# Optimization experiments

Measured on AMD Instinct MI355X. Metric: run time of the kernel, lower is better.

The kernel has to match this reference:

```python
import jax, jax.numpy as jnp
import numpy as np

D = 768; H = 12; HEAD = 6; SD = 64; S1 = SD * (HEAD - 1); S2 = SD * HEAD
HID = 3072; B = 8; N = 1024
SCALE = (D // H) ** -0.5
EPS = 1e-5


def _ln(x, g, b):
    m = jnp.mean(x, axis=-1, keepdims=True)
    v = jnp.var(x, axis=-1, keepdims=True)
    return (x - m) * jax.lax.rsqrt(v + EPS) * g + b


def setup_inputs() -> dict:
    key = jax.random.key(0)
    ks = jax.random.split(key, 20)
    p = lambda k, shape, s=0.02: (jax.random.normal(k, shape, dtype=jnp.float32) * s)
    return {
        "x": jax.random.normal(ks[0], (B, N, D), dtype=jnp.float32),
        # norm1 / norm12 / norm13 (pre-attention split LayerNorms)
        "ln1a_g": jnp.ones((S1,), jnp.float32), "ln1a_b": jnp.zeros((S1,), jnp.float32),
        "ln1b_g": jnp.ones((SD,), jnp.float32), "ln1b_b": jnp.zeros((SD,), jnp.float32),
        "ln1c_g": jnp.ones((D - S2,), jnp.float32), "ln1c_b": jnp.zeros((D - S2,), jnp.float32),
        # norm2 / norm22 / norm23 (pre-MLP split LayerNorms)
        "ln2a_g": jnp.ones((S1,), jnp.float32), "ln2a_b": jnp.zeros((S1,), jnp.float32),
        "ln2b_g": jnp.ones((SD,), jnp.float32), "ln2b_b": jnp.zeros((SD,), jnp.float32),
        "ln2c_g": jnp.ones((D - S2,), jnp.float32), "ln2c_b": jnp.zeros((D - S2,), jnp.float32),
        # attention (qkv has no bias since qkv_bias=False)
        "qkv_w": p(ks[1], (3 * D, D)),
        "proj_w": p(ks[2], (D, D)), "proj_b": jnp.zeros((D,), jnp.float32),
        # mlp
        "fc1_w": p(ks[3], (HID, D)), "fc1_b": jnp.zeros((HID,), jnp.float32),
        "fc2_w": p(ks[4], (D, HID)), "fc2_b": jnp.zeros((D,), jnp.float32),
    }


def _split_norm(x, ga, ba, gb, bb, gc, bc):
    return jnp.concatenate([
        _ln(x[:, :, :S1], ga, ba),
        _ln(x[:, :, S1:S2], gb, bb),
        _ln(x[:, :, S2:], gc, bc),
    ], axis=2)


def _attention(x, qkv_w, proj_w, proj_b):
    Bq, Nq, C = x.shape
    hd = C // H
    qkv = jnp.einsum('bnc,dc->bnd', x, qkv_w)  # [B,N,3C]
    qkv = qkv.reshape(Bq, Nq, 3, H, hd).transpose(2, 0, 3, 1, 4)
    q, k, v = qkv[0], qkv[1], qkv[2]  # [B,H,N,hd]
    attn = jax.nn.softmax(jnp.einsum('bhqd,bhkd->bhqk', q, k) * SCALE, axis=-1)
    y = jnp.einsum('bhqk,bhkd->bhqd', attn, v)  # [B,H,N,hd]
    y = y.transpose(0, 2, 1, 3).reshape(Bq, Nq, C)
    return jnp.einsum('bnc,dc->bnd', y, proj_w) + proj_b


def reference(x, ln1a_g, ln1a_b, ln1b_g, ln1b_b, ln1c_g, ln1c_b,
              ln2a_g, ln2a_b, ln2b_g, ln2b_b, ln2c_g, ln2c_b,
              qkv_w, proj_w, proj_b, fc1_w, fc1_b, fc2_w, fc2_b):
    norm_x = _split_norm(x, ln1a_g, ln1a_b, ln1b_g, ln1b_b, ln1c_g, ln1c_b)
    x = x + _attention(norm_x, qkv_w, proj_w, proj_b)
    norm2_x = _split_norm(x, ln2a_g, ln2a_b, ln2b_g, ln2b_b, ln2c_g, ln2c_b)
    h = jax.nn.gelu(jnp.einsum('bnc,hc->bnh', norm2_x, fc1_w) + fc1_b, approximate=False)
    x = x + (jnp.einsum('bnh,ch->bnc', h, fc2_w) + fc2_b)
    return x
```

## Files before the change

kernel.cpp:

```cpp
#include <hip/hip_runtime.h>
#include <math.h>

#define NTOK 8192
#define DIM 768
#define SEQ 1024
#define NH 12
#define HD 64
#define HID 3072
#define S1V 320
#define S2V 384

typedef unsigned short bfu;
typedef __attribute__((ext_vector_type(8))) short short8;
typedef __attribute__((ext_vector_type(4))) float f32x4;

__device__ __forceinline__ bfu f2bf(float f){
  unsigned int u = __float_as_uint(f);
  u += 0x7FFFu + ((u >> 16) & 1u);
  return (bfu)(u >> 16);
}
__device__ __forceinline__ f32x4 mfma16(short8 a, short8 b, f32x4 c){
  return __builtin_amdgcn_mfma_f32_16x16x32_bf16(a, b, c, 0, 0, 0);
}
__device__ __forceinline__ void gll16(const void* g, void* l){
  __builtin_amdgcn_global_load_lds(
      (const __attribute__((address_space(1))) unsigned int*)g,
      (__attribute__((address_space(3))) unsigned int*)l, 16, 0, 0);
}
__device__ __forceinline__ int swz(int a){ return a ^ (((a >> 7) & 7) << 4); }

__global__ __launch_bounds__(256) void cvt_kernel(const float4* __restrict__ src,
                                                  ushort4* __restrict__ dst, int n4){
  for (int i = blockIdx.x * 256 + threadIdx.x; i < n4; i += gridDim.x * 256){
    float4 f = src[i];
    ushort4 o;
    o.x = f2bf(f.x); o.y = f2bf(f.y); o.z = f2bf(f.z); o.w = f2bf(f.w);
    dst[i] = o;
  }
}

__global__ __launch_bounds__(256) void ln_split(
    const float* __restrict__ x,
    const float* __restrict__ ga, const float* __restrict__ ba,
    const float* __restrict__ gb, const float* __restrict__ bb2,
    const float* __restrict__ gc, const float* __restrict__ bc,
    bfu* __restrict__ out)
{
  const int row = blockIdx.x, t = threadIdx.x;
  const float* xr = x + (size_t)row * DIM;
  const float e0 = xr[t], e1 = xr[t + 256], e2 = xr[t + 512];
  float s0 = e0, q0 = e0 * e0, s1 = 0.f, q1 = 0.f, s2 = e2, q2 = e2 * e2;
  const int i1 = t + 256;
  if (i1 < S1V)      { s0 += e1; q0 += e1 * e1; }
  else if (i1 < S2V) { s1 += e1; q1 += e1 * e1; }
  else               { s2 += e1; q2 += e1 * e1; }
  float v[6] = {s0, q0, s1, q1, s2, q2};
  #pragma unroll
  for (int k = 0; k < 6; ++k)
    #pragma unroll
    for (int off = 32; off; off >>= 1)
      v[k] += __shfl_xor(v[k], off);
  __shared__ float red[6][4];
  const int lane = t & 63, wave = t >> 6;
  if (lane == 0){
    #pragma unroll
    for (int k = 0; k < 6; ++k) red[k][wave] = v[k];
  }
  __syncthreads();
  float tt[6];
  #pragma unroll
  for (int k = 0; k < 6; ++k) tt[k] = red[k][0] + red[k][1] + red[k][2] + red[k][3];
  const float m0 = tt[0] * (1.f/320.f);
  const float r0 = rsqrtf(tt[1] * (1.f/320.f) - m0*m0 + 1e-5f);
  const float m1 = tt[2] * (1.f/64.f);
  const float r1 = rsqrtf(tt[3] * (1.f/64.f) - m1*m1 + 1e-5f);
  const float m2 = tt[4] * (1.f/384.f);
  const float r2 = rsqrtf(tt[5] * (1.f/384.f) - m2*m2 + 1e-5f);
  bfu* orow = out + (size_t)row * DIM;
  orow[t] = f2bf((e0 - m0) * r0 * ga[t] + ba[t]);
  {
    float ov;
    if (i1 < S1V)      ov = (e1 - m0) * r0 * ga[i1] + ba[i1];
    else if (i1 < S2V) ov = (e1 - m1) * r1 * gb[i1 - S1V] + bb2[i1 - S1V];
    else               ov = (e1 - m2) * r2 * gc[i1 - S2V] + bc[i1 - S2V];
    orow[i1] = f2bf(ov);
  }
  const int i2 = t + 512;
  orow[i2] = f2bf((e2 - m2) * r2 * gc[i2 - S2V] + bc[i2 - S2V]);
}

template<int BIAS, int GELU_, int RESID, int OUTF32, int QSC>
__global__ __launch_bounds__(256) void gemm_bt(
    const bfu* __restrict__ A, const bfu* __restrict__ Bw,
    int N, int K, int ntn,
    const float* __restrict__ bias, const float* __restrict__ resid,
    float* __restrict__ outf, bfu* __restrict__ outb)
{
  __shared__ __align__(16) char lds[2][2][8192];
  const int tid = threadIdx.x;
  const int lane = tid & 63;
  const int wave = tid >> 6;
  const int wm = wave >> 1, wn = wave & 1;
  const int tm = blockIdx.x / ntn, tn = blockIdx.x % ntn;
  const int r = lane & 15, g = lane >> 4;

  f32x4 acc[4][4];
  #pragma unroll
  for (int i = 0; i < 4; ++i)
    #pragma unroll
    for (int j = 0; j < 4; ++j) acc[i][j] = (f32x4){0.f, 0.f, 0.f, 0.f};

  int rowS[2], colS[2], Pof[2];
  #pragma unroll
  for (int is = 0; is < 2; ++is){
    const int P = is * 4096 + tid * 16;
    const int L = swz(P);
    Pof[is] = P; rowS[is] = L >> 6; colS[is] = (L & 63) >> 1;
  }
  const bfu* Arow = A  + (size_t)tm * 128 * K;
  const bfu* Brow = Bw + (size_t)tn * 128 * K;

  int offA[4], offB[4];
  #pragma unroll
  for (int f = 0; f < 4; ++f){
    offA[f] = swz((wm * 64 + f * 16 + r) * 64 + g * 16);
    offB[f] = swz((wn * 64 + f * 16 + r) * 64 + g * 16);
  }

  const int nk = K >> 5;
  #pragma unroll
  for (int is = 0; is < 2; ++is){
    gll16(Arow + (size_t)rowS[is] * K + colS[is], &lds[0][0][Pof[is]]);
    gll16(Brow + (size_t)rowS[is] * K + colS[is], &lds[0][1][Pof[is]]);
  }
  __syncthreads();

  for (int t = 0; t < nk; ++t){
    const int cur = t & 1;
    if (t + 1 < nk){
      const int k0 = (t + 1) << 5;
      #pragma unroll
      for (int is = 0; is < 2; ++is){
        gll16(Arow + (size_t)rowS[is] * K + k0 + colS[is], &lds[cur ^ 1][0][Pof[is]]);
        gll16(Brow + (size_t)rowS[is] * K + k0 + colS[is], &lds[cur ^ 1][1][Pof[is]]);
      }
    }
    const char* lA = lds[cur][0];
    const char* lB = lds[cur][1];
    short8 af[4], bfv[4];
    #pragma unroll
    for (int f = 0; f < 4; ++f){
      af[f]  = *(const short8*)(lA + offA[f]);
      bfv[f] = *(const short8*)(lB + offB[f]);
    }
    #pragma unroll
    for (int i = 0; i < 4; ++i)
      #pragma unroll
      for (int j = 0; j < 4; ++j)
        acc[i][j] = mfma16(af[i], bfv[j], acc[i][j]);
    __syncthreads();
  }

  const int row0 = tm * 128 + wm * 64;
  const int col0 = tn * 128 + wn * 64;
  #pragma unroll
  for (int j = 0; j < 4; ++j){
    const int colb = col0 + j * 16 + r;
    const float bi = BIAS ? bias[colb] : 0.f;
    #pragma unroll
    for (int i = 0; i < 4; ++i){
      #pragma unroll
      for (int q = 0; q < 4; ++q){
        const int rowg = row0 + i * 16 + g * 4 + q;
        float v = acc[i][j][q] + bi;
        if (GELU_) v = 0.5f * v * (1.f + erff(v * 0.70710678118654752440f));
        if (QSC && colb < 768) v *= 0.125f;
        const size_t idx = (size_t)rowg * N + colb;
        if (RESID) v += resid[idx];
        if (OUTF32) outf[idx] = v;
        else        outb[idx] = f2bf(v);
      }
    }
  }
}

__global__ __launch_bounds__(256) void vtrans(const bfu* __restrict__ qkv, bfu* __restrict__ vt){
  __shared__ bfu tile[64][66];
  const int bh = blockIdx.x, kt = blockIdx.y;
  const int b = bh / NH, h = bh - b * NH;
  const int tid = threadIdx.x;
  const int tr = tid >> 5;
  const int tc = (tid & 31) * 2;
  #pragma unroll
  for (int pass = 0; pass < 8; ++pass){
    const int k = pass * 8 + tr;
    const bfu* src = qkv + (size_t)(b * SEQ + kt * 64 + k) * 2304 + 1536 + h * 64 + tc;
    tile[k][tc] = src[0]; tile[k][tc + 1] = src[1];
  }
  __syncthreads();
  #pragma unroll
  for (int pass = 0; pass < 8; ++pass){
    const int d = pass * 8 + tr;
    bfu* dst = vt + ((size_t)bh * 64 + d) * SEQ + kt * 64 + tc;
    dst[0] = tile[tc][d]; dst[1] = tile[tc + 1][d];
  }
}

__global__ __launch_bounds__(512) void attn2(
    const bfu* __restrict__ qkv, const bfu* __restrict__ vt, bfu* __restrict__ y)
{
  __shared__ __align__(16) char kbuf[2][8192];
  __shared__ __align__(16) char vbuf[2][8192];
  __shared__ __align__(16) char plds_all[8][2048];
  const int tid = threadIdx.x, lane = tid & 63, wave = tid >> 6;
  char* plds = plds_all[wave];
  const int blk = blockIdx.x;
  const int bh = blk >> 3, q128 = blk & 7;
  const int b = bh / NH, h = bh - b * NH;
  const int r = lane & 15, g = lane >> 4;

  const bfu* qbase = qkv + (size_t)(b * SEQ + q128 * 128 + wave * 16 + r) * 2304 + h * 64;
  const short8 qf0 = *(const short8*)(qbase + g * 8);
  const short8 qf1 = *(const short8*)(qbase + 32 + g * 8);

  const int P = tid * 16;
  const int Ls = swz(P);
  const int srow = Ls >> 7, scol = Ls & 127;
  const char* kg = (const char*)(qkv + (size_t)(b * SEQ) * 2304 + 768 + h * 64)
                   + (size_t)srow * 4608 + scol;
  const char* vg = (const char*)(vt + (size_t)bh * 64 * SEQ)
                   + (size_t)srow * 2048 + scol;

  int off[4][2];
  #pragma unroll
  for (int f = 0; f < 4; ++f){
    off[f][0] = swz((f * 16 + r) * 128 + g * 16);
    off[f][1] = swz((f * 16 + r) * 128 + 64 + g * 16);
  }

  float m_[4], l_[4];
  f32x4 yacc[4];
  #pragma unroll
  for (int i = 0; i < 4; ++i){ m_[i] = -1e30f; l_[i] = 0.f; yacc[i] = (f32x4){0.f,0.f,0.f,0.f}; }

  gll16(kg, &kbuf[0][P]);
  gll16(vg, &vbuf[0][P]);
  __syncthreads();

  for (int kt = 0; kt < 16; ++kt){
    const int cur = kt & 1;
    if (kt + 1 < 16){
      gll16(kg + (size_t)(kt + 1) * 294912, &kbuf[cur ^ 1][P]);
      gll16(vg + (kt + 1) * 128, &vbuf[cur ^ 1][P]);
    }
    const char* lK = kbuf[cur];
    const char* lV = vbuf[cur];

    f32x4 s[4];
    #pragma unroll
    for (int c = 0; c < 4; ++c){
      const short8 kf0 = *(const short8*)(lK + off[c][0]);
      const short8 kf1 = *(const short8*)(lK + off[c][1]);
      s[c] = (f32x4){0.f, 0.f, 0.f, 0.f};
      s[c] = mfma16(qf0, kf0, s[c]);
      s[c] = mfma16(qf1, kf1, s[c]);
    }
    float pm[4];
    #pragma unroll
    for (int q = 0; q < 4; ++q)
      pm[q] = fmaxf(fmaxf(s[0][q], s[1][q]), fmaxf(s[2][q], s[3][q]));
    #pragma unroll
    for (int q = 0; q < 4; ++q)
      #pragma unroll
      for (int o = 1; o < 16; o <<= 1)
        pm[q] = fmaxf(pm[q], __shfl_xor(pm[q], o));
    float rs[4];
    #pragma unroll
    for (int q = 0; q < 4; ++q){
      const float mn = fmaxf(m_[q], pm[q]);
      const float al = __expf(m_[q] - mn);
      m_[q] = mn;
      l_[q] *= al;
      #pragma unroll
      for (int f = 0; f < 4; ++f) yacc[f][q] *= al;
      float acc = 0.f;
      #pragma unroll
      for (int c = 0; c < 4; ++c){
        const float p = __expf(s[c][q] - mn);
        s[c][q] = p;
        acc += p;
      }
      rs[q] = acc;
    }
    #pragma unroll
    for (int q = 0; q < 4; ++q){
      #pragma unroll
      for (int o = 1; o < 16; o <<= 1)
        rs[q] += __shfl_xor(rs[q], o);
      l_[q] += rs[q];
    }
    #pragma unroll
    for (int c = 0; c < 4; ++c)
      #pragma unroll
      for (int q = 0; q < 4; ++q){
        const int a = swz((g * 4 + q) * 128 + (c * 16 + r) * 2);
        *(bfu*)&plds[a] = f2bf(s[c][q]);
      }
    short8 pa[2];
    #pragma unroll
    for (int ks = 0; ks < 2; ++ks)
      pa[ks] = *(const short8*)&plds[swz(r * 128 + ks * 64 + g * 16)];
    #pragma unroll
    for (int f = 0; f < 4; ++f){
      const short8 vf0 = *(const short8*)(lV + off[f][0]);
      const short8 vf1 = *(const short8*)(lV + off[f][1]);
      yacc[f] = mfma16(pa[0], vf0, yacc[f]);
      yacc[f] = mfma16(pa[1], vf1, yacc[f]);
    }
    __syncthreads();
  }

  bfu* yb = y + (size_t)(b * SEQ + q128 * 128 + wave * 16) * DIM + h * 64;
  #pragma unroll
  for (int f = 0; f < 4; ++f)
    #pragma unroll
    for (int q = 0; q < 4; ++q)
      yb[(size_t)(g * 4 + q) * DIM + f * 16 + r] = f2bf(yacc[f][q] / l_[q]);
}

extern "C" void kernel_launch(void* const* d_in, const int* in_sizes, int n_in,
                              void* d_out, int out_size, void* d_ws, size_t ws_size,
                              hipStream_t stream) {
  const float* x      = (const float*)d_in[0];
  const float* ln1ag  = (const float*)d_in[1];
  const float* ln1ab  = (const float*)d_in[2];
  const float* ln1bg  = (const float*)d_in[3];
  const float* ln1bb  = (const float*)d_in[4];
  const float* ln1cg  = (const float*)d_in[5];
  const float* ln1cb  = (const float*)d_in[6];
  const float* ln2ag  = (const float*)d_in[7];
  const float* ln2ab  = (const float*)d_in[8];
  const float* ln2bg  = (const float*)d_in[9];
  const float* ln2bb  = (const float*)d_in[10];
  const float* ln2cg  = (const float*)d_in[11];
  const float* ln2cb  = (const float*)d_in[12];
  const float* qkv_w  = (const float*)d_in[13];
  const float* proj_w = (const float*)d_in[14];
  const float* proj_b = (const float*)d_in[15];
  const float* fc1_w  = (const float*)d_in[16];
  const float* fc1_b  = (const float*)d_in[17];
  const float* fc2_w  = (const float*)d_in[18];
  const float* fc2_b  = (const float*)d_in[19];
  float* outp = (float*)d_out;

  char* ws = (char*)d_ws;
  bfu* wqkv   = (bfu*)(ws + 0);
  bfu* wproj  = (bfu*)(ws + 3538944);
  bfu* wfc1   = (bfu*)(ws + 4718592);
  bfu* wfc2   = (bfu*)(ws + 9437184);
  bfu* lnbuf  = (bfu*)(ws + 14155776);
  bfu* ybuf   = (bfu*)(ws + 26738688);
  bfu* qkvbuf = (bfu*)(ws + 39321600);
  bfu* vtbuf  = (bfu*)(ws + 77070336);
  bfu* hbuf   = qkvbuf;

  cvt_kernel<<<512, 256, 0, stream>>>((const float4*)qkv_w,  (ushort4*)wqkv, 2304*768/4);
  cvt_kernel<<<256, 256, 0, stream>>>((const float4*)proj_w, (ushort4*)wproj, 768*768/4);
  cvt_kernel<<<512, 256, 0, stream>>>((const float4*)fc1_w,  (ushort4*)wfc1, 3072*768/4);
  cvt_kernel<<<512, 256, 0, stream>>>((const float4*)fc2_w,  (ushort4*)wfc2, 768*3072/4);

  ln_split<<<NTOK, 256, 0, stream>>>(x, ln1ag, ln1ab, ln1bg, ln1bb, ln1cg, ln1cb, lnbuf);
  gemm_bt<0,0,0,0,1><<<64*18, 256, 0, stream>>>(lnbuf, wqkv, 2304, 768, 18,
                                                nullptr, nullptr, nullptr, qkvbuf);
  vtrans<<<dim3(96,16), 256, 0, stream>>>(qkvbuf, vtbuf);
  attn2<<<768, 512, 0, stream>>>(qkvbuf, vtbuf, ybuf);
  gemm_bt<1,0,1,1,0><<<64*6, 256, 0, stream>>>(ybuf, wproj, 768, 768, 6,
                                               proj_b, x, outp, nullptr);
  ln_split<<<NTOK, 256, 0, stream>>>(outp, ln2ag, ln2ab, ln2bg, ln2bb, ln2cg, ln2cb, lnbuf);
  gemm_bt<1,1,0,0,0><<<64*24, 256, 0, stream>>>(lnbuf, wfc1, 3072, 768, 24,
                                                fc1_b, nullptr, nullptr, hbuf);
  gemm_bt<1,0,1,1,0><<<64*6, 256, 0, stream>>>(hbuf, wfc2, 768, 3072, 6,
                                               fc2_b, outp, outp, nullptr);
}
```

Measured before the change: 454.4 us.

## Replace 128x128 GEMM with 256x256 tile kernel, XCD swizzle, split-K atomics for fc2

Replaces the 128x128 K=32 GEMM with a 512-thread kernel using 256x256 tiles and K=64 steps. Loads are issued two stages ahead with explicit vmcnt waits, and MFMA sections get s_setprio. Block indices are remapped across the 8 XCDs, and fc2 splits K in two and accumulates into the output with atomicAdd, relying on outp already holding the residual. This targets better data reuse and MFMA density. The risks are higher LDS and register pressure and fewer blocks, for example 96 blocks for proj, plus nondeterministic atomic float adds.

Result: slower. 503.3 us (+10.8%).

```diff
diff --git a/kernel.cpp b/kernel.cpp
--- a/kernel.cpp
+++ b/kernel.cpp
@@ -28,6 +28,7 @@
       (__attribute__((address_space(3))) unsigned int*)l, 16, 0, 0);
 }
 __device__ __forceinline__ int swz(int a){ return a ^ (((a >> 7) & 7) << 4); }
+__device__ __forceinline__ int swz2(int a){ return a ^ (((a >> 7) & 7) << 4); }
 
 __global__ __launch_bounds__(256) void cvt_kernel(const float4* __restrict__ src,
                                                   ushort4* __restrict__ dst, int n4){
@@ -89,96 +90,119 @@
   orow[i2] = f2bf((e2 - m2) * r2 * gc[i2 - S2V] + bc[i2 - S2V]);
 }
 
-template<int BIAS, int GELU_, int RESID, int OUTF32, int QSC>
-__global__ __launch_bounds__(256) void gemm_bt(
+template<int BIAS, int GELU_, int RESID, int OUTF32, int QSC, int SPLITK>
+__global__ __launch_bounds__(512, 2) void gemm256(
     const bfu* __restrict__ A, const bfu* __restrict__ Bw,
-    int N, int K, int ntn,
+    int N, int ldK, int ntn,
     const float* __restrict__ bias, const float* __restrict__ resid,
     float* __restrict__ outf, bfu* __restrict__ outb)
 {
-  __shared__ __align__(16) char lds[2][2][8192];
+  __shared__ __align__(16) char lds[2][2][32768];
   const int tid = threadIdx.x;
   const int lane = tid & 63;
   const int wave = tid >> 6;
-  const int wm = wave >> 1, wn = wave & 1;
-  const int tm = blockIdx.x / ntn, tn = blockIdx.x % ntn;
+  const int wm = wave >> 2, wn = wave & 3;
   const int r = lane & 15, g = lane >> 4;
-
-  f32x4 acc[4][4];
-  #pragma unroll
-  for (int i = 0; i < 4; ++i)
+  const int sx = (r & 7) << 4;
+
+  const int nwg = gridDim.x, cpx = nwg >> 3;
+  const int sb = (blockIdx.x & 7) * cpx + (blockIdx.x >> 3);
+  const int per = 32 * ntn;
+  const int kg  = SPLITK ? (sb / per) : 0;
+  const int rem = SPLITK ? (sb % per) : sb;
+  const int tm = rem / ntn, tn = rem % ntn;
+
+  const int Kloc = SPLITK ? (ldK >> 1) : ldK;
+  const size_t ld2 = (size_t)ldK * 2;
+  const size_t koff2 = (size_t)kg * Kloc * 2;
+
+  f32x4 acc[8][4];
+  #pragma unroll
+  for (int i = 0; i < 8; ++i)
     #pragma unroll
     for (int j = 0; j < 4; ++j) acc[i][j] = (f32x4){0.f, 0.f, 0.f, 0.f};
 
-  int rowS[2], colS[2], Pof[2];
-  #pragma unroll
-  for (int is = 0; is < 2; ++is){
-    const int P = is * 4096 + tid * 16;
-    const int L = swz(P);
-    Pof[is] = P; rowS[is] = L >> 6; colS[is] = (L & 63) >> 1;
-  }
-  const bfu* Arow = A  + (size_t)tm * 128 * K;
-  const bfu* Brow = Bw + (size_t)tn * 128 * K;
-
-  int offA[4], offB[4];
-  #pragma unroll
-  for (int f = 0; f < 4; ++f){
-    offA[f] = swz((wm * 64 + f * 16 + r) * 64 + g * 16);
-    offB[f] = swz((wn * 64 + f * 16 + r) * 64 + g * 16);
-  }
-
-  const int nk = K >> 5;
-  #pragma unroll
-  for (int is = 0; is < 2; ++is){
-    gll16(Arow + (size_t)rowS[is] * K + colS[is], &lds[0][0][Pof[is]]);
-    gll16(Brow + (size_t)rowS[is] * K + colS[is], &lds[0][1][Pof[is]]);
-  }
-  __syncthreads();
-
-  for (int t = 0; t < nk; ++t){
+  const int Ls = swz2(tid * 16);
+  const int r0 = Ls >> 7;
+  const int c0 = Ls & 127;
+  const char* Abase = (const char*)A + (size_t)tm * 256 * ld2 + koff2 + c0;
+  const char* Bbase = (const char*)Bw + (size_t)tn * 256 * ld2 + koff2 + c0;
+  const int tid16 = tid * 16;
+
+  const int nt = Kloc >> 6;
+
+  #define STAGE(b, t) do { \
+    const char* Ao = Abase + (size_t)(t) * 128; \
+    const char* Bo = Bbase + (size_t)(t) * 128; \
+    _Pragma("unroll") \
+    for (int is = 0; is < 4; ++is) \
+      gll16(Ao + (size_t)(is * 64 + r0) * ld2, &lds[b][0][is * 8192 + tid16]); \
+    _Pragma("unroll") \
+    for (int is = 0; is < 4; ++is) \
+      gll16(Bo + (size_t)(is * 64 + r0) * ld2, &lds[b][1][is * 8192 + tid16]); \
+  } while (0)
+
+  STAGE(0, 0);
+  STAGE(1, 1);
+  asm volatile("s_waitcnt vmcnt(8)" ::: "memory");
+  __builtin_amdgcn_s_barrier();
+
+  for (int t = 0; t < nt; ++t){
     const int cur = t & 1;
-    if (t + 1 < nk){
-      const int k0 = (t + 1) << 5;
-      #pragma unroll
-      for (int is = 0; is < 2; ++is){
-        gll16(Arow + (size_t)rowS[is] * K + k0 + colS[is], &lds[cur ^ 1][0][Pof[is]]);
-        gll16(Brow + (size_t)rowS[is] * K + k0 + colS[is], &lds[cur ^ 1][1][Pof[is]]);
-      }
-    }
     const char* lA = lds[cur][0];
     const char* lB = lds[cur][1];
-    short8 af[4], bfv[4];
-    #pragma unroll
-    for (int f = 0; f < 4; ++f){
-      af[f]  = *(const short8*)(lA + offA[f]);
-      bfv[f] = *(const short8*)(lB + offB[f]);
-    }
-    #pragma unroll
-    for (int i = 0; i < 4; ++i)
-      #pragma unroll
-      for (int j = 0; j < 4; ++j)
-        acc[i][j] = mfma16(af[i], bfv[j], acc[i][j]);
-    __syncthreads();
-  }
-
-  const int row0 = tm * 128 + wm * 64;
-  const int col0 = tn * 128 + wn * 64;
-  #pragma unroll
-  for (int j = 0; j < 4; ++j){
-    const int colb = col0 + j * 16 + r;
-    const float bi = BIAS ? bias[colb] : 0.f;
-    #pragma unroll
-    for (int i = 0; i < 4; ++i){
+    short8 bfr[4][2];
+    #pragma unroll
+    for (int n = 0; n < 4; ++n)
+      #pragma unroll
+      for (int h = 0; h < 2; ++h)
+        bfr[n][h] = *(const short8*)(lB + ((((wn * 64 + n * 16 + r) * 128) + h * 64 + g * 16) ^ sx));
+    #pragma unroll
+    for (int mp = 0; mp < 4; ++mp){
+      short8 afr[2][2];
+      #pragma unroll
+      for (int mm = 0; mm < 2; ++mm)
+        #pragma unroll
+        for (int h = 0; h < 2; ++h)
+          afr[mm][h] = *(const short8*)(lA + ((((wm * 128 + (mp * 2 + mm) * 16 + r) * 128) + h * 64 + g * 16) ^ sx));
+      __builtin_amdgcn_s_setprio(1);
+      #pragma unroll
+      for (int mm = 0; mm < 2; ++mm)
+        #pragma unroll
+        for (int n = 0; n < 4; ++n){
+          acc[mp * 2 + mm][n] = mfma16(afr[mm][0], bfr[n][0], acc[mp * 2 + mm][n]);
+          acc[mp * 2 + mm][n] = mfma16(afr[mm][1], bfr[n][1], acc[mp * 2 + mm][n]);
+        }
+      __builtin_amdgcn_s_setprio(0);
+    }
+    asm volatile("s_waitcnt vmcnt(0)" ::: "memory");
+    __builtin_amdgcn_s_barrier();
+    if (t + 2 < nt) STAGE(cur, t + 2);
+  }
+  #undef STAGE
+
+  const int row0 = tm * 256 + wm * 128;
+  const int col0 = tn * 256 + wn * 64;
+  #pragma unroll
+  for (int n = 0; n < 4; ++n){
+    const int colb = col0 + n * 16 + r;
+    const float bi = (BIAS && (!SPLITK || kg == 0)) ? bias[colb] : 0.f;
+    #pragma unroll
+    for (int m = 0; m < 8; ++m){
       #pragma unroll
       for (int q = 0; q < 4; ++q){
-        const int rowg = row0 + i * 16 + g * 4 + q;
-        float v = acc[i][j][q] + bi;
+        const int rowg = row0 + m * 16 + g * 4 + q;
+        float v = acc[m][n][q] + bi;
         if (GELU_) v = 0.5f * v * (1.f + erff(v * 0.70710678118654752440f));
         if (QSC && colb < 768) v *= 0.125f;
         const size_t idx = (size_t)rowg * N + colb;
-        if (RESID) v += resid[idx];
-        if (OUTF32) outf[idx] = v;
-        else        outb[idx] = f2bf(v);
+        if (SPLITK){
+          atomicAdd(&outf[idx], v);
+        } else {
+          if (RESID) v += resid[idx];
+          if (OUTF32) outf[idx] = v;
+          else        outb[idx] = f2bf(v);
+        }
       }
     }
   }
@@ -370,15 +394,15 @@
   cvt_kernel<<<512, 256, 0, stream>>>((const float4*)fc2_w,  (ushort4*)wfc2, 768*3072/4);
 
   ln_split<<<NTOK, 256, 0, stream>>>(x, ln1ag, ln1ab, ln1bg, ln1bb, ln1cg, ln1cb, lnbuf);
-  gemm_bt<0,0,0,0,1><<<64*18, 256, 0, stream>>>(lnbuf, wqkv, 2304, 768, 18,
+  gemm256<0,0,0,0,1,0><<<288, 512, 0, stream>>>(lnbuf, wqkv, 2304, 768, 9,
                                                 nullptr, nullptr, nullptr, qkvbuf);
   vtrans<<<dim3(96,16), 256, 0, stream>>>(qkvbuf, vtbuf);
   attn2<<<768, 512, 0, stream>>>(qkvbuf, vtbuf, ybuf);
-  gemm_bt<1,0,1,1,0><<<64*6, 256, 0, stream>>>(ybuf, wproj, 768, 768, 6,
+  gemm256<1,0,1,1,0,0><<<96, 512, 0, stream>>>(ybuf, wproj, 768, 768, 3,
                                                proj_b, x, outp, nullptr);
   ln_split<<<NTOK, 256, 0, stream>>>(outp, ln2ag, ln2ab, ln2bg, ln2bb, ln2cg, ln2cb, lnbuf);
-  gemm_bt<1,1,0,0,0><<<64*24, 256, 0, stream>>>(lnbuf, wfc1, 3072, 768, 24,
+  gemm256<1,1,0,0,0,0><<<384, 512, 0, stream>>>(lnbuf, wfc1, 3072, 768, 12,
                                                 fc1_b, nullptr, nullptr, hbuf);
-  gemm_bt<1,0,1,1,0><<<64*6, 256, 0, stream>>>(hbuf, wfc2, 768, 3072, 6,
-                                               fc2_b, outp, outp, nullptr);
-}
+  gemm256<1,0,0,0,0,1><<<192, 512, 0, stream>>>(hbuf, wfc2, 768, 3072, 3,
+                                                fc2_b, nullptr, outp, nullptr);
+}
```

## Use smaller M tiles for N=768 GEMMs, swizzle block order, fuse weight casts

Applied to the files above, without the earlier changes.

Templates the GEMM core on tile shape. The proj and fc2 GEMMs (N=768) now use 64x128 tiles, doubling their block count from 384 to 768 so more of the GPU stays busy. Block indices are remapped in groups of 8 (an XCD-style swizzle) to change which tiles run together and improve cache locality. The four weight-conversion launches are merged into one kernel to cut launch overhead. Smaller tiles lower per-block data reuse, and the remap assumes the grid size is divisible by 8.

Result: no change. 457.0 us (+0.6%).

```diff
diff --git a/kernel.cpp b/kernel.cpp
--- a/kernel.cpp
+++ b/kernel.cpp
@@ -29,13 +29,23 @@
 }
 __device__ __forceinline__ int swz(int a){ return a ^ (((a >> 7) & 7) << 4); }
 
-__global__ __launch_bounds__(256) void cvt_kernel(const float4* __restrict__ src,
-                                                  ushort4* __restrict__ dst, int n4){
-  for (int i = blockIdx.x * 256 + threadIdx.x; i < n4; i += gridDim.x * 256){
-    float4 f = src[i];
+__global__ __launch_bounds__(256) void cvt_all(
+    const float4* __restrict__ s0, ushort4* __restrict__ d0,
+    const float4* __restrict__ s1, ushort4* __restrict__ d1,
+    const float4* __restrict__ s2, ushort4* __restrict__ d2,
+    const float4* __restrict__ s3, ushort4* __restrict__ d3)
+{
+  const int total = 1769472;
+  for (int i = blockIdx.x * 256 + threadIdx.x; i < total; i += gridDim.x * 256){
+    const float4* s; ushort4* d; int j = i;
+    if (j < 442368)       { s = s0; d = d0; }
+    else if (j < 589824)  { s = s1; d = d1; j -= 442368; }
+    else if (j < 1179648) { s = s2; d = d2; j -= 589824; }
+    else                  { s = s3; d = d3; j -= 1179648; }
+    float4 f = s[j];
     ushort4 o;
     o.x = f2bf(f.x); o.y = f2bf(f.y); o.z = f2bf(f.z); o.w = f2bf(f.w);
-    dst[i] = o;
+    d[j] = o;
   }
 }
 
@@ -89,86 +99,99 @@
   orow[i2] = f2bf((e2 - m2) * r2 * gc[i2 - S2V] + bc[i2 - S2V]);
 }
 
-template<int BIAS, int GELU_, int RESID, int OUTF32, int QSC>
-__global__ __launch_bounds__(256) void gemm_bt(
+template<int FM, int FN, int BIAS, int GELU_, int RESID, int OUTF32, int QSC>
+__device__ __forceinline__ void gemm_core(
     const bfu* __restrict__ A, const bfu* __restrict__ Bw,
     int N, int K, int ntn,
     const float* __restrict__ bias, const float* __restrict__ resid,
     float* __restrict__ outf, bfu* __restrict__ outb)
 {
-  __shared__ __align__(16) char lds[2][2][8192];
+  constexpr int BM = FM * 32, BN = FN * 32;
+  constexpr int ABYTES = BM * 64, BBYTES = BN * 64;
+  constexpr int AISS = ABYTES / 4096, BISS = BBYTES / 4096;
+  __shared__ __align__(16) char lA_[2][ABYTES];
+  __shared__ __align__(16) char lB_[2][BBYTES];
   const int tid = threadIdx.x;
   const int lane = tid & 63;
   const int wave = tid >> 6;
   const int wm = wave >> 1, wn = wave & 1;
-  const int tm = blockIdx.x / ntn, tn = blockIdx.x % ntn;
   const int r = lane & 15, g = lane >> 4;
 
-  f32x4 acc[4][4];
-  #pragma unroll
-  for (int i = 0; i < 4; ++i)
-    #pragma unroll
-    for (int j = 0; j < 4; ++j) acc[i][j] = (f32x4){0.f, 0.f, 0.f, 0.f};
-
-  int rowS[2], colS[2], Pof[2];
-  #pragma unroll
-  for (int is = 0; is < 2; ++is){
-    const int P = is * 4096 + tid * 16;
-    const int L = swz(P);
-    Pof[is] = P; rowS[is] = L >> 6; colS[is] = (L & 63) >> 1;
-  }
-  const bfu* Arow = A  + (size_t)tm * 128 * K;
-  const bfu* Brow = Bw + (size_t)tn * 128 * K;
-
-  int offA[4], offB[4];
-  #pragma unroll
-  for (int f = 0; f < 4; ++f){
-    offA[f] = swz((wm * 64 + f * 16 + r) * 64 + g * 16);
-    offB[f] = swz((wn * 64 + f * 16 + r) * 64 + g * 16);
-  }
+  const int nwg = gridDim.x, cpx = nwg >> 3;
+  const int sb = (blockIdx.x & 7) * cpx + (blockIdx.x >> 3);
+  const int tm = sb / ntn, tn = sb % ntn;
+  const size_t ld2 = (size_t)K * 2;
+
+  f32x4 acc[FM][FN];
+  #pragma unroll
+  for (int i = 0; i < FM; ++i)
+    #pragma unroll
+    for (int j = 0; j < FN; ++j) acc[i][j] = (f32x4){0.f, 0.f, 0.f, 0.f};
+
+  int PofA[AISS], rowA[AISS], colA[AISS];
+  #pragma unroll
+  for (int is = 0; is < AISS; ++is){
+    const int P = is * 4096 + tid * 16, L = swz(P);
+    PofA[is] = P; rowA[is] = L >> 6; colA[is] = L & 63;
+  }
+  int PofB[BISS], rowB[BISS], colB[BISS];
+  #pragma unroll
+  for (int is = 0; is < BISS; ++is){
+    const int P = is * 4096 + tid * 16, L = swz(P);
+    PofB[is] = P; rowB[is] = L >> 6; colB[is] = L & 63;
+  }
+  const char* Abase = (const char*)A + (size_t)tm * BM * ld2;
+  const char* Bbase = (const char*)Bw + (size_t)tn * BN * ld2;
+
+  int offA[FM], offB[FN];
+  #pragma unroll
+  for (int f = 0; f < FM; ++f) offA[f] = swz((wm * FM * 16 + f * 16 + r) * 64 + g * 16);
+  #pragma unroll
+  for (int f = 0; f < FN; ++f) offB[f] = swz((wn * FN * 16 + f * 16 + r) * 64 + g * 16);
 
   const int nk = K >> 5;
   #pragma unroll
-  for (int is = 0; is < 2; ++is){
-    gll16(Arow + (size_t)rowS[is] * K + colS[is], &lds[0][0][Pof[is]]);
-    gll16(Brow + (size_t)rowS[is] * K + colS[is], &lds[0][1][Pof[is]]);
-  }
+  for (int is = 0; is < AISS; ++is)
+    gll16(Abase + (size_t)rowA[is] * ld2 + colA[is], &lA_[0][PofA[is]]);
+  #pragma unroll
+  for (int is = 0; is < BISS; ++is)
+    gll16(Bbase + (size_t)rowB[is] * ld2 + colB[is], &lB_[0][PofB[is]]);
   __syncthreads();
 
   for (int t = 0; t < nk; ++t){
     const int cur = t & 1;
     if (t + 1 < nk){
-      const int k0 = (t + 1) << 5;
-      #pragma unroll
-      for (int is = 0; is < 2; ++is){
-        gll16(Arow + (size_t)rowS[is] * K + k0 + colS[is], &lds[cur ^ 1][0][Pof[is]]);
-        gll16(Brow + (size_t)rowS[is] * K + k0 + colS[is], &lds[cur ^ 1][1][Pof[is]]);
-      }
-    }
-    const char* lA = lds[cur][0];
-    const char* lB = lds[cur][1];
-    short8 af[4], bfv[4];
-    #pragma unroll
-    for (int f = 0; f < 4; ++f){
-      af[f]  = *(const short8*)(lA + offA[f]);
-      bfv[f] = *(const short8*)(lB + offB[f]);
-    }
-    #pragma unroll
-    for (int i = 0; i < 4; ++i)
-      #pragma unroll
-      for (int j = 0; j < 4; ++j)
-        acc[i][j] = mfma16(af[i], bfv[j], acc[i][j]);
+      const int kb = (t + 1) * 64;
+      #pragma unroll
+      for (int is = 0; is < AISS; ++is)
+        gll16(Abase + (size_t)rowA[is] * ld2 + kb + colA[is], &lA_[cur ^ 1][PofA[is]]);
+      #pragma unroll
+      for (int is = 0; is < BISS; ++is)
+        gll16(Bbase + (size_t)rowB[is] * ld2 + kb + colB[is], &lB_[cur ^ 1][PofB[is]]);
+    }
+    const char* lA = lA_[cur];
+    const char* lB = lB_[cur];
+    short8 af[FM], bf[FN];
+    #pragma unroll
+    for (int f = 0; f < FM; ++f) af[f] = *(const short8*)(lA + offA[f]);
+    #pragma unroll
+    for (int f = 0; f < FN; ++f) bf[f] = *(const short8*)(lB + offB[f]);
+    #pragma unroll
+    for (int i = 0; i < FM; ++i)
+      #pragma unroll
+      for (int j = 0; j < FN; ++j)
+        acc[i][j] = mfma16(af[i], bf[j], acc[i][j]);
     __syncthreads();
   }
 
-  const int row0 = tm * 128 + wm * 64;
-  const int col0 = tn * 128 + wn * 64;
-  #pragma unroll
-  for (int j = 0; j < 4; ++j){
+  const int row0 = tm * BM + wm * FM * 16;
+  const int col0 = tn * BN + wn * FN * 16;
+  #pragma unroll
+  for (int j = 0; j < FN; ++j){
     const int colb = col0 + j * 16 + r;
     const float bi = BIAS ? bias[colb] : 0.f;
     #pragma unroll
-    for (int i = 0; i < 4; ++i){
+    for (int i = 0; i < FM; ++i){
       #pragma unroll
       for (int q = 0; q < 4; ++q){
         const int rowg = row0 + i * 16 + g * 4 + q;
@@ -182,6 +205,22 @@
       }
     }
   }
+}
+
+__global__ __launch_bounds__(256) void gemm_qkv(const bfu* A, const bfu* Bw, bfu* out){
+  gemm_core<4,4,0,0,0,0,1>(A, Bw, 2304, 768, 18, nullptr, nullptr, nullptr, out);
+}
+__global__ __launch_bounds__(256) void gemm_proj(const bfu* A, const bfu* Bw,
+                                                 const float* bias, const float* resid, float* out){
+  gemm_core<2,4,1,0,1,1,0>(A, Bw, 768, 768, 6, bias, resid, out, nullptr);
+}
+__global__ __launch_bounds__(256) void gemm_fc1(const bfu* A, const bfu* Bw,
+                                                const float* bias, bfu* out){
+  gemm_core<4,4,1,1,0,0,0>(A, Bw, 3072, 768, 24, bias, nullptr, nullptr, out);
+}
+__global__ __launch_bounds__(256) void gemm_fc2(const bfu* A, const bfu* Bw,
+                                                const float* bias, float* out){
+  gemm_core<2,4,1,0,1,1,0>(A, Bw, 768, 3072, 6, bias, out, out, nullptr);
 }
 
 __global__ __launch_bounds__(256) void vtrans(const bfu* __restrict__ qkv, bfu* __restrict__ vt){
@@ -364,21 +403,17 @@
   bfu* vtbuf  = (bfu*)(ws + 77070336);
   bfu* hbuf   = qkvbuf;
 
-  cvt_kernel<<<512, 256, 0, stream>>>((const float4*)qkv_w,  (ushort4*)wqkv, 2304*768/4);
-  cvt_kernel<<<256, 256, 0, stream>>>((const float4*)proj_w, (ushort4*)wproj, 768*768/4);
-  cvt_kernel<<<512, 256, 0, stream>>>((const float4*)fc1_w,  (ushort4*)wfc1, 3072*768/4);
-  cvt_kernel<<<512, 256, 0, stream>>>((const float4*)fc2_w,  (ushort4*)wfc2, 768*3072/4);
+  cvt_all<<<2048, 256, 0, stream>>>((const float4*)qkv_w,  (ushort4*)wqkv,
+                                    (const float4*)proj_w, (ushort4*)wproj,
+                                    (const float4*)fc1_w,  (ushort4*)wfc1,
+                                    (const float4*)fc2_w,  (ushort4*)wfc2);
 
   ln_split<<<NTOK, 256, 0, stream>>>(x, ln1ag, ln1ab, ln1bg, ln1bb, ln1cg, ln1cb, lnbuf);
-  gemm_bt<0,0,0,0,1><<<64*18, 256, 0, stream>>>(lnbuf, wqkv, 2304, 768, 18,
-                                                nullptr, nullptr, nullptr, qkvbuf);
+  gemm_qkv<<<1152, 256, 0, stream>>>(lnbuf, wqkv, qkvbuf);
   vtrans<<<dim3(96,16), 256, 0, stream>>>(qkvbuf, vtbuf);
   attn2<<<768, 512, 0, stream>>>(qkvbuf, vtbuf, ybuf);
-  gemm_bt<1,0,1,1,0><<<64*6, 256, 0, stream>>>(ybuf, wproj, 768, 768, 6,
-                                               proj_b, x, outp, nullptr);
+  gemm_proj<<<768, 256, 0, stream>>>(ybuf, wproj, proj_b, x, outp);
   ln_split<<<NTOK, 256, 0, stream>>>(outp, ln2ag, ln2ab, ln2bg, ln2bb, ln2cg, ln2cb, lnbuf);
-  gemm_bt<1,1,0,0,0><<<64*24, 256, 0, stream>>>(lnbuf, wfc1, 3072, 768, 24,
-                                                fc1_b, nullptr, nullptr, hbuf);
-  gemm_bt<1,0,1,1,0><<<64*6, 256, 0, stream>>>(hbuf, wfc2, 768, 3072, 6,
-                                               fc2_b, outp, outp, nullptr);
-}
+  gemm_fc1<<<1536, 256, 0, stream>>>(lnbuf, wfc1, fc1_b, hbuf);
+  gemm_fc2<<<768, 256, 0, stream>>>(hbuf, wfc2, fc2_b, outp);
+}
```
